# Kernel optimization log

Measured on AMD Instinct MI355X. Metric: run time of the kernel, lower is better.

## Reference

```python
import jax, jax.numpy as jnp
import numpy as np


def derived_adjustedmean(activation_in, carry_in):
    # avnn.derives.derived_adjustedmean: per-sample scalar derived from the
    # activator and carry channels. Assumed: average of the two channel means.
    return 0.5 * (jnp.mean(activation_in, axis=-1) + jnp.mean(carry_in, axis=-1))


def setup_inputs() -> dict:
    key = jax.random.key(0)
    k1, k2, k3 = jax.random.split(key, 3)
    B, D_IN, D_OUT = 2048, 4096, 4096
    x = jax.random.normal(k1, (B, D_IN, 2), dtype=jnp.float32)
    # nn.Linear default init scale ~ 1/sqrt(fan_in)
    scale = 1.0 / np.sqrt(D_IN)
    W = jax.random.uniform(k2, (D_OUT, D_IN), dtype=jnp.float32, minval=-scale, maxval=scale)
    b = jax.random.uniform(k3, (D_OUT,), dtype=jnp.float32, minval=-scale, maxval=scale)
    return {"x": x, "W": W, "b": b}


def reference(x, W, b):
    # x: [B, D_in, 2] -> channel 0 = activator, channel 1 = carry
    activation_in = x[..., 0]           # [B, D_in]
    carry_in = x[..., 1]                # [B, D_in]
    # Linear + ReLU on the activator channel
    activation_out = jax.nn.relu(jnp.einsum('bi,oi->bo', activation_in, W) + b)  # [B, D_out]
    # Vectorized replacement of the per-batch Python loop: per-row scalar derive,
    # broadcast-filled across the output features.
    val = derived_adjustedmean(activation_in, carry_in)            # [B]
    carry_out = jnp.broadcast_to(val[:, None], activation_out.shape)  # [B, D_out]
    return jnp.stack([activation_out, carry_out], axis=-1)         # [B, D_out, 2]
```

## Files before the change

kernel.cpp:

```cpp
#include <hip/hip_runtime.h>
#include <stdint.h>


typedef __bf16 bf16x8_t __attribute__((ext_vector_type(8)));
typedef float f32x4_t __attribute__((ext_vector_type(4)));
typedef __attribute__((address_space(1))) void gvoid_t;
typedef __attribute__((address_space(3))) void lvoid_t;

__device__ __forceinline__ uint32_t f32_to_bf16_rne(float f) {
    uint32_t u = __float_as_uint(f);
    return (u + 0x7fffu + ((u >> 16) & 1u)) >> 16;
}

__device__ __forceinline__ uint32_t swz(uint32_t b) {
    return b ^ (((b >> 7) & 7u) << 4);
}

__device__ __forceinline__ bf16x8_t ds_read128(uint32_t addr) {
    bf16x8_t d;
    asm volatile("ds_read_b128 %0, %1" : "=&v"(d) : "v"(addr));
    return d;
}

__global__ __launch_bounds__(256) void convert_x_stats(
    const float4* __restrict__ x4,
    uint32_t* __restrict__ abf,
    float* __restrict__ val, int din) {
    const int row = blockIdx.x;
    const int t = threadIdx.x;
    const int f4pr = din >> 1;
    const float4* xr = x4 + (size_t)row * f4pr;
    float s = 0.f;
    if (abf != nullptr) {
        uint32_t* ar = abf + ((size_t)row * din >> 1);
        for (int i = t; i < f4pr; i += 256) {
            float4 v = xr[i];
            s += (v.x + v.y) + (v.z + v.w);
            ar[i] = f32_to_bf16_rne(v.x) | (f32_to_bf16_rne(v.z) << 16);
        }
    } else {
        for (int i = t; i < f4pr; i += 256) {
            float4 v = xr[i];
            s += (v.x + v.y) + (v.z + v.w);
        }
    }
#pragma unroll
    for (int off = 32; off; off >>= 1) s += __shfl_down(s, off, 64);
    __shared__ float red[4];
    if ((t & 63) == 0) red[t >> 6] = s;
    __syncthreads();
    if (t == 0) val[row] = (red[0] + red[1] + red[2] + red[3]) / (float)(2 * din);
}

__global__ __launch_bounds__(256) void convert_w(
    const float4* __restrict__ w4, uint2* __restrict__ wbf, int n4) {
    const int i = blockIdx.x * 256 + threadIdx.x;
    if (i < n4) {
        float4 v = w4[i];
        uint2 p;
        p.x = f32_to_bf16_rne(v.x) | (f32_to_bf16_rne(v.y) << 16);
        p.y = f32_to_bf16_rne(v.z) | (f32_to_bf16_rne(v.w) << 16);
        wbf[i] = p;
    }
}

#define BKB 128
#define A_SLAB 16384
#define B_SLAB 32768
#define B_BASE (3 * A_SLAB)
#define LDS_BYTES (B_BASE + 3 * B_SLAB)

__global__ __launch_bounds__(512, 2) void gemm8p(
    const uint16_t* __restrict__ Abf, const uint16_t* __restrict__ Wbf,
    const float* __restrict__ bias, const float* __restrict__ val,
    float* __restrict__ out, int M, int N, int K) {
    extern __shared__ char lds[];
    const uint32_t lds0 = (uint32_t)(uintptr_t)(lvoid_t*)lds;

    const int tid = threadIdx.x;
    const int wv = tid >> 6;
    const int lane = tid & 63;
    const int lrow = lane & 15, lkg = lane >> 4;
    const int m0 = blockIdx.y * 128;
    const int n0 = blockIdx.x * 256;
    const int wr = wv >> 2, wc = wv & 3;

    uint32_t asrc[2], bsrc[4];
#pragma unroll
    for (int l = 0; l < 2; ++l) {
        uint32_t sb = swz((uint32_t)(l * 512 + tid) * 16u);
        asrc[l] = (uint32_t)(m0 + (int)(sb >> 7)) * (uint32_t)(K * 2) + (sb & 127u);
    }
#pragma unroll
    for (int l = 0; l < 4; ++l) {
        uint32_t sb = swz((uint32_t)(l * 512 + tid) * 16u);
        bsrc[l] = (uint32_t)(n0 + (int)(sb >> 7)) * (uint32_t)(K * 2) + (sb & 127u);
    }
    uint32_t ard[4], brd[4];
#pragma unroll
    for (int m = 0; m < 4; ++m)
        ard[m] = swz((uint32_t)(wr * 64 + m * 16 + lrow) * 128u + (uint32_t)(lkg * 16));
#pragma unroll
    for (int n = 0; n < 4; ++n)
        brd[n] = swz((uint32_t)(wc * 64 + n * 16 + lrow) * 128u + (uint32_t)(lkg * 16));

    f32x4_t acc[4][4];
#pragma unroll
    for (int i = 0; i < 4; ++i)
#pragma unroll
        for (int j = 0; j < 4; ++j) acc[i][j] = (f32x4_t){0.f, 0.f, 0.f, 0.f};

    const int NT = K >> 6;

    auto STAGE = [&](int tt) {
        const int slot = tt % 3;
#pragma unroll
        for (int l = 0; l < 2; ++l) {
            const char* src = (const char*)Abf + asrc[l] + (size_t)tt * BKB;
            char* dst = lds + slot * A_SLAB + (l * 512 + wv * 64) * 16;
            __builtin_amdgcn_global_load_lds((gvoid_t*)src, (lvoid_t*)dst, 16, 0, 0);
        }
#pragma unroll
        for (int l = 0; l < 4; ++l) {
            const char* src = (const char*)Wbf + bsrc[l] + (size_t)tt * BKB;
            char* dst = lds + B_BASE + slot * B_SLAB + (l * 512 + wv * 64) * 16;
            __builtin_amdgcn_global_load_lds((gvoid_t*)src, (lvoid_t*)dst, 16, 0, 0);
        }
    };

    STAGE(0);
    if (NT > 1) STAGE(1);
    asm volatile("s_waitcnt vmcnt(6)" ::: "memory");
    __builtin_amdgcn_sched_barrier(0);
    __builtin_amdgcn_s_barrier();

    for (int t = 0; t < NT; ++t) {
        const int slot = t % 3;
        const uint32_t la = lds0 + slot * A_SLAB;
        const uint32_t lb = lds0 + B_BASE + slot * B_SLAB;
        bf16x8_t af0[4], bf0[4], af1[4], bf1[4];
#pragma unroll
        for (int m = 0; m < 4; ++m) af0[m] = ds_read128(la + ard[m]);
#pragma unroll
        for (int n = 0; n < 4; ++n) bf0[n] = ds_read128(lb + brd[n]);
#pragma unroll
        for (int m = 0; m < 4; ++m) af1[m] = ds_read128(la + (ard[m] ^ 64u));
#pragma unroll
        for (int n = 0; n < 4; ++n) bf1[n] = ds_read128(lb + (brd[n] ^ 64u));
        if (t + 2 < NT) STAGE(t + 2);
        asm volatile("s_waitcnt lgkmcnt(8)" ::: "memory");
        __builtin_amdgcn_sched_barrier(0);
        __builtin_amdgcn_s_setprio(1);
#pragma unroll
        for (int m = 0; m < 4; ++m)
#pragma unroll
            for (int n = 0; n < 4; ++n)
                acc[m][n] = __builtin_amdgcn_mfma_f32_16x16x32_bf16(af0[m], bf0[n],
                                                                    acc[m][n], 0, 0, 0);
        __builtin_amdgcn_s_setprio(0);
        asm volatile("s_waitcnt lgkmcnt(0)" ::: "memory");
        __builtin_amdgcn_sched_barrier(0);
        __builtin_amdgcn_s_setprio(1);
#pragma unroll
        for (int m = 0; m < 4; ++m)
#pragma unroll
            for (int n = 0; n < 4; ++n)
                acc[m][n] = __builtin_amdgcn_mfma_f32_16x16x32_bf16(af1[m], bf1[n],
                                                                    acc[m][n], 0, 0, 0);
        __builtin_amdgcn_s_setprio(0);
        if (t < NT - 1) {
            if (t + 2 < NT) { asm volatile("s_waitcnt vmcnt(6)" ::: "memory"); }
            else            { asm volatile("s_waitcnt vmcnt(0)" ::: "memory"); }
            __builtin_amdgcn_sched_barrier(0);
            __builtin_amdgcn_s_barrier();
        }
    }

    const int gmb = m0 + wr * 64;
    const int gnb = n0 + wc * 64;
    float bcol[4];
#pragma unroll
    for (int n = 0; n < 4; ++n) bcol[n] = bias[gnb + n * 16 + lrow];
#pragma unroll
    for (int m = 0; m < 4; ++m) {
#pragma unroll
        for (int r = 0; r < 4; ++r) {
            const int row = gmb + m * 16 + lkg * 4 + r;
            const float vr = val[row];
            float2* orow = (float2*)(out + (size_t)row * N * 2);
#pragma unroll
            for (int n = 0; n < 4; ++n) {
                const int col = gnb + n * 16 + lrow;
                float a = fmaxf(acc[m][n][r] + bcol[n], 0.f);
                orow[col] = make_float2(a, vr);
            }
        }
    }
}

__global__ __launch_bounds__(256) void gemm_fallback(
    const float* __restrict__ xf, const float* __restrict__ Wf,
    const float* __restrict__ bias, const float* __restrict__ val,
    float* __restrict__ out, int M, int N, int K) {
    __shared__ uint16_t lA[128 * 32];
    __shared__ uint16_t lB[128 * 32];
    const int tid = threadIdx.x;
    const int wv = tid >> 6;
    const int lane = tid & 63;
    const int lrow = lane & 15;
    const int lkg = lane >> 4;
    const int m0 = blockIdx.y * 128;
    const int n0 = blockIdx.x * 128;
    const int wr = wv >> 1, wc = wv & 1;
    f32x4_t acc[4][4];
#pragma unroll
    for (int i = 0; i < 4; ++i)
#pragma unroll
        for (int j = 0; j < 4; ++j) acc[i][j] = (f32x4_t){0.f, 0.f, 0.f, 0.f};
    for (int k0 = 0; k0 < K; k0 += 32) {
        float4 va[8];
        float4 vb[4];
#pragma unroll
        for (int i = 0; i < 8; ++i) {
            const int p = i * 256 + tid;
            const int row = p >> 4, pc = p & 15;
            va[i] = *(const float4*)(xf + ((size_t)(m0 + row) * K + k0 + pc * 2) * 2);
        }
#pragma unroll
        for (int i = 0; i < 4; ++i) {
            const int q = i * 256 + tid;
            const int row = q >> 3, qc = q & 7;
            vb[i] = *(const float4*)(Wf + (size_t)(n0 + row) * K + k0 + qc * 4);
        }
        __syncthreads();
#pragma unroll
        for (int i = 0; i < 8; ++i) {
            const int p = i * 256 + tid;
            const int row = p >> 4, pc = p & 15;
            *(uint32_t*)&lA[row * 32 + pc * 2] =
                f32_to_bf16_rne(va[i].x) | (f32_to_bf16_rne(va[i].z) << 16);
        }
#pragma unroll
        for (int i = 0; i < 4; ++i) {
            const int q = i * 256 + tid;
            const int row = q >> 3, qc = q & 7;
            uint2 pk;
            pk.x = f32_to_bf16_rne(vb[i].x) | (f32_to_bf16_rne(vb[i].y) << 16);
            pk.y = f32_to_bf16_rne(vb[i].z) | (f32_to_bf16_rne(vb[i].w) << 16);
            *(uint2*)&lB[row * 32 + qc * 4] = pk;
        }
        __syncthreads();
        bf16x8_t af[4], bfr[4];
#pragma unroll
        for (int i = 0; i < 4; ++i)
            af[i] = *(const bf16x8_t*)&lA[(wr * 64 + i * 16 + lrow) * 32 + lkg * 8];
#pragma unroll
        for (int j = 0; j < 4; ++j)
            bfr[j] = *(const bf16x8_t*)&lB[(wc * 64 + j * 16 + lrow) * 32 + lkg * 8];
#pragma unroll
        for (int i = 0; i < 4; ++i)
#pragma unroll
            for (int j = 0; j < 4; ++j)
                acc[i][j] = __builtin_amdgcn_mfma_f32_16x16x32_bf16(af[i], bfr[j],
                                                                    acc[i][j], 0, 0, 0);
        __syncthreads();
    }
    const int gm = m0 + wr * 64;
    const int gn = n0 + wc * 64;
    float bcol[4];
#pragma unroll
    for (int j = 0; j < 4; ++j) bcol[j] = bias[gn + j * 16 + lrow];
#pragma unroll
    for (int i = 0; i < 4; ++i) {
#pragma unroll
        for (int r = 0; r < 4; ++r) {
            const int row = gm + i * 16 + lkg * 4 + r;
            const float vr = val[row];
            float2* orow = (float2*)(out + (size_t)row * N * 2);
#pragma unroll
            for (int j = 0; j < 4; ++j) {
                const int col = gn + j * 16 + lrow;
                float a = fmaxf(acc[i][j][r] + bcol[j], 0.f);
                orow[col] = make_float2(a, vr);
            }
        }
    }
}

extern "C" void kernel_launch(void* const* d_in, const int* in_sizes, int n_in,
                              void* d_out, int out_size, void* d_ws, size_t ws_size,
                              hipStream_t stream) {
    const float* x = (const float*)d_in[0];
    const float* W = (const float*)d_in[1];
    const float* b = (const float*)d_in[2];
    float* out = (float*)d_out;

    const int DOUT = in_sizes[2];
    const int DIN = in_sizes[1] / DOUT;
    const int B = in_sizes[0] / (2 * DIN);

    float* val = (float*)d_ws;
    const size_t aoff = 8192;
    const size_t abytes = (size_t)B * DIN * 2;
    const size_t wbytes = (size_t)DOUT * DIN * 2;
    const bool big = ws_size >= aoff + abytes + wbytes &&
                     (B % 128) == 0 && (DOUT % 256) == 0 && (DIN % 128) == 0;

    if (big) {
        uint32_t* abf = (uint32_t*)((char*)d_ws + aoff);
        uint32_t* wbf = (uint32_t*)((char*)d_ws + aoff + abytes);
        convert_x_stats<<<B, 256, 0, stream>>>((const float4*)x, abf, val, DIN);
        const int n4 = DOUT * DIN / 4;
        convert_w<<<(n4 + 255) / 256, 256, 0, stream>>>((const float4*)W, (uint2*)wbf, n4);
        (void)hipFuncSetAttribute((const void*)gemm8p,
                                  hipFuncAttributeMaxDynamicSharedMemorySize, LDS_BYTES);
        dim3 grid(DOUT / 256, B / 128);
        gemm8p<<<grid, 512, LDS_BYTES, stream>>>((const uint16_t*)abf, (const uint16_t*)wbf,
                                                 b, val, out, B, DOUT, DIN);
    } else {
        convert_x_stats<<<B, 256, 0, stream>>>((const float4*)x, nullptr, val, DIN);
        dim3 grid(DOUT / 128, B / 128);
        gemm_fallback<<<grid, 256, 0, stream>>>(x, W, b, val, out, B, DOUT, DIN);
    }
}
```

Measured before the change: 105.5 us.

## Shrink GEMM tile to 128x128 with 4 waves and double buffering

Replaces the 8-wave 128x256 block tile with a 4-wave 128x128 tile and cuts the LDS pipeline from triple to double buffering. The next stage's prefetch is now issued before the LDS reads, and the loop waits on vmcnt(0) at every iteration. The aim is a smaller per-block LDS footprint and more blocks in flight across CUs. In exchange each block reuses less data, so global and L2 traffic per FLOP rises, and the shallower pipeline exposes more memory latency.

```diff
diff --git a/kernel.cpp b/kernel.cpp
--- a/kernel.cpp
+++ b/kernel.cpp
@@ -66,11 +66,11 @@
 
 #define BKB 128
 #define A_SLAB 16384
-#define B_SLAB 32768
-#define B_BASE (3 * A_SLAB)
-#define LDS_BYTES (B_BASE + 3 * B_SLAB)
-
-__global__ __launch_bounds__(512, 2) void gemm8p(
+#define B_SLAB 16384
+#define B_BASE (2 * A_SLAB)
+#define LDS_BYTES (B_BASE + 2 * B_SLAB)
+
+__global__ __launch_bounds__(256, 2) void gemm2b(
     const uint16_t* __restrict__ Abf, const uint16_t* __restrict__ Wbf,
     const float* __restrict__ bias, const float* __restrict__ val,
     float* __restrict__ out, int M, int N, int K) {
@@ -82,18 +82,14 @@
     const int lane = tid & 63;
     const int lrow = lane & 15, lkg = lane >> 4;
     const int m0 = blockIdx.y * 128;
-    const int n0 = blockIdx.x * 256;
-    const int wr = wv >> 2, wc = wv & 3;
-
-    uint32_t asrc[2], bsrc[4];
-#pragma unroll
-    for (int l = 0; l < 2; ++l) {
-        uint32_t sb = swz((uint32_t)(l * 512 + tid) * 16u);
+    const int n0 = blockIdx.x * 128;
+    const int wr = wv >> 1, wc = wv & 1;
+
+    uint32_t asrc[4], bsrc[4];
+#pragma unroll
+    for (int l = 0; l < 4; ++l) {
+        uint32_t sb = swz((uint32_t)(l * 256 + tid) * 16u);
         asrc[l] = (uint32_t)(m0 + (int)(sb >> 7)) * (uint32_t)(K * 2) + (sb & 127u);
-    }
-#pragma unroll
-    for (int l = 0; l < 4; ++l) {
-        uint32_t sb = swz((uint32_t)(l * 512 + tid) * 16u);
         bsrc[l] = (uint32_t)(n0 + (int)(sb >> 7)) * (uint32_t)(K * 2) + (sb & 127u);
     }
     uint32_t ard[4], brd[4];
@@ -113,31 +109,27 @@
     const int NT = K >> 6;
 
     auto STAGE = [&](int tt) {
-        const int slot = tt % 3;
-#pragma unroll
-        for (int l = 0; l < 2; ++l) {
-            const char* src = (const char*)Abf + asrc[l] + (size_t)tt * BKB;
-            char* dst = lds + slot * A_SLAB + (l * 512 + wv * 64) * 16;
-            __builtin_amdgcn_global_load_lds((gvoid_t*)src, (lvoid_t*)dst, 16, 0, 0);
-        }
+        const int slot = tt & 1;
 #pragma unroll
         for (int l = 0; l < 4; ++l) {
-            const char* src = (const char*)Wbf + bsrc[l] + (size_t)tt * BKB;
-            char* dst = lds + B_BASE + slot * B_SLAB + (l * 512 + wv * 64) * 16;
-            __builtin_amdgcn_global_load_lds((gvoid_t*)src, (lvoid_t*)dst, 16, 0, 0);
+            const char* srcA = (const char*)Abf + asrc[l] + (size_t)tt * BKB;
+            char* dstA = lds + slot * A_SLAB + l * 4096 + wv * 1024;
+            __builtin_amdgcn_global_load_lds((gvoid_t*)srcA, (lvoid_t*)dstA, 16, 0, 0);
+            const char* srcB = (const char*)Wbf + bsrc[l] + (size_t)tt * BKB;
+            char* dstB = lds + B_BASE + slot * B_SLAB + l * 4096 + wv * 1024;
+            __builtin_amdgcn_global_load_lds((gvoid_t*)srcB, (lvoid_t*)dstB, 16, 0, 0);
         }
     };
 
     STAGE(0);
-    if (NT > 1) STAGE(1);
-    asm volatile("s_waitcnt vmcnt(6)" ::: "memory");
+    asm volatile("s_waitcnt vmcnt(0)" ::: "memory");
     __builtin_amdgcn_sched_barrier(0);
     __builtin_amdgcn_s_barrier();
 
     for (int t = 0; t < NT; ++t) {
-        const int slot = t % 3;
-        const uint32_t la = lds0 + slot * A_SLAB;
-        const uint32_t lb = lds0 + B_BASE + slot * B_SLAB;
+        const uint32_t la = lds0 + (t & 1) * A_SLAB;
+        const uint32_t lb = lds0 + B_BASE + (t & 1) * B_SLAB;
+        if (t + 1 < NT) STAGE(t + 1);
         bf16x8_t af0[4], bf0[4], af1[4], bf1[4];
 #pragma unroll
         for (int m = 0; m < 4; ++m) af0[m] = ds_read128(la + ard[m]);
@@ -147,7 +139,6 @@
         for (int m = 0; m < 4; ++m) af1[m] = ds_read128(la + (ard[m] ^ 64u));
 #pragma unroll
         for (int n = 0; n < 4; ++n) bf1[n] = ds_read128(lb + (brd[n] ^ 64u));
-        if (t + 2 < NT) STAGE(t + 2);
         asm volatile("s_waitcnt lgkmcnt(8)" ::: "memory");
         __builtin_amdgcn_sched_barrier(0);
         __builtin_amdgcn_s_setprio(1);
@@ -168,9 +159,8 @@
                 acc[m][n] = __builtin_amdgcn_mfma_f32_16x16x32_bf16(af1[m], bf1[n],
                                                                     acc[m][n], 0, 0, 0);
         __builtin_amdgcn_s_setprio(0);
-        if (t < NT - 1) {
-            if (t + 2 < NT) { asm volatile("s_waitcnt vmcnt(6)" ::: "memory"); }
-            else            { asm volatile("s_waitcnt vmcnt(0)" ::: "memory"); }
+        if (t + 1 < NT) {
+            asm volatile("s_waitcnt vmcnt(0)" ::: "memory");
             __builtin_amdgcn_sched_barrier(0);
             __builtin_amdgcn_s_barrier();
         }
@@ -304,7 +294,7 @@
     const size_t abytes = (size_t)B * DIN * 2;
     const size_t wbytes = (size_t)DOUT * DIN * 2;
     const bool big = ws_size >= aoff + abytes + wbytes &&
-                     (B % 128) == 0 && (DOUT % 256) == 0 && (DIN % 128) == 0;
+                     (B % 128) == 0 && (DOUT % 128) == 0 && (DIN % 64) == 0;
 
     if (big) {
         uint32_t* abf = (uint32_t*)((char*)d_ws + aoff);
@@ -312,10 +302,10 @@
         convert_x_stats<<<B, 256, 0, stream>>>((const float4*)x, abf, val, DIN);
         const int n4 = DOUT * DIN / 4;
         convert_w<<<(n4 + 255) / 256, 256, 0, stream>>>((const float4*)W, (uint2*)wbf, n4);
-        (void)hipFuncSetAttribute((const void*)gemm8p,
+        (void)hipFuncSetAttribute((const void*)gemm2b,
                                   hipFuncAttributeMaxDynamicSharedMemorySize, LDS_BYTES);
-        dim3 grid(DOUT / 256, B / 128);
-        gemm8p<<<grid, 512, LDS_BYTES, stream>>>((const uint16_t*)abf, (const uint16_t*)wbf,
+        dim3 grid(DOUT / 128, B / 128);
+        gemm2b<<<grid, 256, LDS_BYTES, stream>>>((const uint16_t*)abf, (const uint16_t*)wbf,
                                                  b, val, out, B, DOUT, DIN);
     } else {
         convert_x_stats<<<B, 256, 0, stream>>>((const float4*)x, nullptr, val, DIN);
```

New measurement: 99.53 us. -5.6%, faster.

## Split GEMM K-tile into two barrier-synchronized phases with interleaved staging

Applied to the files above, without the earlier changes.

Each K-tile of the bf16 MFMA GEMM main loop is split into two half-K phases. Each phase loads its own fragments from LDS, issues part of the next-next tile's global-to-LDS copies (A plus one W chunk, then the remaining W chunks), and runs 16 MFMAs between two workgroup barriers. Launch bounds drop from 2 to 1 workgroups per SIMD-occupancy hint, which frees more registers per thread. The goal is to spread global loads evenly and keep all waves in lockstep so they overlap better with compute. The cost is four barriers per tile instead of one, and the kernel may lose occupancy from the lower hint.

```diff
diff --git a/kernel.cpp b/kernel.cpp
--- a/kernel.cpp
+++ b/kernel.cpp
@@ -70,7 +70,7 @@
 #define B_BASE (3 * A_SLAB)
 #define LDS_BYTES (B_BASE + 3 * B_SLAB)
 
-__global__ __launch_bounds__(512, 2) void gemm8p(
+__global__ __launch_bounds__(512, 1) void gemm_ph(
     const uint16_t* __restrict__ Abf, const uint16_t* __restrict__ Wbf,
     const float* __restrict__ bias, const float* __restrict__ val,
     float* __restrict__ out, int M, int N, int K) {
@@ -112,69 +112,82 @@
 
     const int NT = K >> 6;
 
-    auto STAGE = [&](int tt) {
-        const int slot = tt % 3;
-#pragma unroll
-        for (int l = 0; l < 2; ++l) {
-            const char* src = (const char*)Abf + asrc[l] + (size_t)tt * BKB;
-            char* dst = lds + slot * A_SLAB + (l * 512 + wv * 64) * 16;
-            __builtin_amdgcn_global_load_lds((gvoid_t*)src, (lvoid_t*)dst, 16, 0, 0);
-        }
-#pragma unroll
-        for (int l = 0; l < 4; ++l) {
-            const char* src = (const char*)Wbf + bsrc[l] + (size_t)tt * BKB;
-            char* dst = lds + B_BASE + slot * B_SLAB + (l * 512 + wv * 64) * 16;
-            __builtin_amdgcn_global_load_lds((gvoid_t*)src, (lvoid_t*)dst, 16, 0, 0);
-        }
-    };
-
-    STAGE(0);
-    if (NT > 1) STAGE(1);
-    asm volatile("s_waitcnt vmcnt(6)" ::: "memory");
-    __builtin_amdgcn_sched_barrier(0);
+#define STAGE_P0(tt)                                                          \
+    {                                                                         \
+        const int slot = (tt) % 3;                                            \
+        _Pragma("unroll") for (int l = 0; l < 2; ++l) {                       \
+            const char* src = (const char*)Abf + asrc[l] + (size_t)(tt) * BKB;\
+            char* dst = lds + slot * A_SLAB + (l * 512 + wv * 64) * 16;       \
+            __builtin_amdgcn_global_load_lds((gvoid_t*)src, (lvoid_t*)dst,    \
+                                             16, 0, 0);                       \
+        }                                                                     \
+        {                                                                     \
+            const char* src = (const char*)Wbf + bsrc[0] + (size_t)(tt) * BKB;\
+            char* dst = lds + B_BASE + slot * B_SLAB + (wv * 64) * 16;        \
+            __builtin_amdgcn_global_load_lds((gvoid_t*)src, (lvoid_t*)dst,    \
+                                             16, 0, 0);                       \
+        }                                                                     \
+    }
+#define STAGE_P1(tt)                                                          \
+    {                                                                         \
+        const int slot = (tt) % 3;                                            \
+        _Pragma("unroll") for (int l = 1; l < 4; ++l) {                       \
+            const char* src = (const char*)Wbf + bsrc[l] + (size_t)(tt) * BKB;\
+            char* dst = lds + B_BASE + slot * B_SLAB + (l * 512 + wv * 64) * 16;\
+            __builtin_amdgcn_global_load_lds((gvoid_t*)src, (lvoid_t*)dst,    \
+                                             16, 0, 0);                       \
+        }                                                                     \
+    }
+#define PHASE(la, lb, ksx, STAGE_CODE, TAIL_CODE)                             \
+    {                                                                         \
+        bf16x8_t af[4], bfr[4];                                               \
+        _Pragma("unroll") for (int m = 0; m < 4; ++m)                         \
+            af[m] = ds_read128((la) + (ard[m] ^ (ksx)));                      \
+        _Pragma("unroll") for (int n = 0; n < 4; ++n)                         \
+            bfr[n] = ds_read128((lb) + (brd[n] ^ (ksx)));                     \
+        STAGE_CODE;                                                           \
+        __builtin_amdgcn_s_barrier();                                         \
+        asm volatile("s_waitcnt lgkmcnt(0)" ::: "memory");                    \
+        __builtin_amdgcn_sched_barrier(0);                                    \
+        __builtin_amdgcn_s_setprio(1);                                        \
+        _Pragma("unroll") for (int m = 0; m < 4; ++m)                         \
+            _Pragma("unroll") for (int n = 0; n < 4; ++n)                     \
+                acc[m][n] = __builtin_amdgcn_mfma_f32_16x16x32_bf16(          \
+                    af[m], bfr[n], acc[m][n], 0, 0, 0);                       \
+        __builtin_amdgcn_s_setprio(0);                                        \
+        TAIL_CODE;                                                            \
+        __builtin_amdgcn_s_barrier();                                         \
+    }
+#define WAIT6  { asm volatile("s_waitcnt vmcnt(6)" ::: "memory");             \
+                 __builtin_amdgcn_sched_barrier(0); }
+#define WAIT0  { asm volatile("s_waitcnt vmcnt(0)" ::: "memory");             \
+                 __builtin_amdgcn_sched_barrier(0); }
+
+    STAGE_P0(0); STAGE_P1(0);
+    if (NT > 1) { STAGE_P0(1); STAGE_P1(1); }
+    if (NT > 1) { WAIT6; } else { WAIT0; }
     __builtin_amdgcn_s_barrier();
 
     for (int t = 0; t < NT; ++t) {
         const int slot = t % 3;
         const uint32_t la = lds0 + slot * A_SLAB;
         const uint32_t lb = lds0 + B_BASE + slot * B_SLAB;
-        bf16x8_t af0[4], bf0[4], af1[4], bf1[4];
-#pragma unroll
-        for (int m = 0; m < 4; ++m) af0[m] = ds_read128(la + ard[m]);
-#pragma unroll
-        for (int n = 0; n < 4; ++n) bf0[n] = ds_read128(lb + brd[n]);
-#pragma unroll
-        for (int m = 0; m < 4; ++m) af1[m] = ds_read128(la + (ard[m] ^ 64u));
-#pragma unroll
-        for (int n = 0; n < 4; ++n) bf1[n] = ds_read128(lb + (brd[n] ^ 64u));
-        if (t + 2 < NT) STAGE(t + 2);
-        asm volatile("s_waitcnt lgkmcnt(8)" ::: "memory");
-        __builtin_amdgcn_sched_barrier(0);
-        __builtin_amdgcn_s_setprio(1);
-#pragma unroll
-        for (int m = 0; m < 4; ++m)
-#pragma unroll
-            for (int n = 0; n < 4; ++n)
-                acc[m][n] = __builtin_amdgcn_mfma_f32_16x16x32_bf16(af0[m], bf0[n],
-                                                                    acc[m][n], 0, 0, 0);
-        __builtin_amdgcn_s_setprio(0);
-        asm volatile("s_waitcnt lgkmcnt(0)" ::: "memory");
-        __builtin_amdgcn_sched_barrier(0);
-        __builtin_amdgcn_s_setprio(1);
-#pragma unroll
-        for (int m = 0; m < 4; ++m)
-#pragma unroll
-            for (int n = 0; n < 4; ++n)
-                acc[m][n] = __builtin_amdgcn_mfma_f32_16x16x32_bf16(af1[m], bf1[n],
-                                                                    acc[m][n], 0, 0, 0);
-        __builtin_amdgcn_s_setprio(0);
-        if (t < NT - 1) {
-            if (t + 2 < NT) { asm volatile("s_waitcnt vmcnt(6)" ::: "memory"); }
-            else            { asm volatile("s_waitcnt vmcnt(0)" ::: "memory"); }
-            __builtin_amdgcn_sched_barrier(0);
-            __builtin_amdgcn_s_barrier();
-        }
-    }
+        if (t + 2 < NT) {
+            PHASE(la, lb, 0u, STAGE_P0(t + 2), );
+            PHASE(la, lb, 64u, STAGE_P1(t + 2), WAIT6);
+        } else if (t + 1 < NT) {
+            PHASE(la, lb, 0u, , );
+            PHASE(la, lb, 64u, , WAIT0);
+        } else {
+            PHASE(la, lb, 0u, , );
+            PHASE(la, lb, 64u, , );
+        }
+    }
+#undef PHASE
+#undef STAGE_P0
+#undef STAGE_P1
+#undef WAIT6
+#undef WAIT0
 
     const int gmb = m0 + wr * 64;
     const int gnb = n0 + wc * 64;
@@ -312,11 +325,12 @@
         convert_x_stats<<<B, 256, 0, stream>>>((const float4*)x, abf, val, DIN);
         const int n4 = DOUT * DIN / 4;
         convert_w<<<(n4 + 255) / 256, 256, 0, stream>>>((const float4*)W, (uint2*)wbf, n4);
-        (void)hipFuncSetAttribute((const void*)gemm8p,
+        (void)hipFuncSetAttribute((const void*)gemm_ph,
                                   hipFuncAttributeMaxDynamicSharedMemorySize, LDS_BYTES);
         dim3 grid(DOUT / 256, B / 128);
-        gemm8p<<<grid, 512, LDS_BYTES, stream>>>((const uint16_t*)abf, (const uint16_t*)wbf,
-                                                 b, val, out, B, DOUT, DIN);
+        gemm_ph<<<grid, 512, LDS_BYTES, stream>>>((const uint16_t*)abf,
+                                                  (const uint16_t*)wbf,
+                                                  b, val, out, B, DOUT, DIN);
     } else {
         convert_x_stats<<<B, 256, 0, stream>>>((const float4*)x, nullptr, val, DIN);
         dim3 grid(DOUT / 128, B / 128);
```

Result: slower. 115.7 us (+9.7%).
